# Optimization experiments

Hardware: AMD Instinct MI355X
Metric: run time of the kernel (lower is better)

The kernel has to match this reference:

```python
import jax, jax.numpy as jnp
import numpy as np

C = 80          # NUM_CLASSES
D = 8525        # total anchors over FPN levels (640 input: 80^2+40^2+20^2+10^2+5^2)
B = 64
EPS = 1e-6


def setup_inputs() -> dict:
    key = jax.random.key(0)
    ks = jax.random.split(key, 8)
    outs = jax.random.normal(ks[0], (B, D, C + 5), dtype=jnp.float32)
    grids = jax.random.uniform(ks[1], (D, 2), dtype=jnp.float32) * 640.0  # anchor centers (px)
    # --- build gres = [gcls(C), centerness(1), g_ltrb(4), mask_pp(1), mask_pos(1), pad(1)] ---
    labels = jax.random.randint(ks[2], (B, D), 0, C)
    mask_pos = (jax.random.uniform(ks[3], (B, D)) < 0.10).astype(jnp.float32)  # in-box positives
    mask_pp = (jax.random.uniform(ks[4], (B, D)) < 0.05).astype(jnp.float32)   # center-radius positives
    gcls = jax.nn.one_hot(labels, C, dtype=jnp.float32) * mask_pos[..., None]
    gcenterness = jax.random.uniform(ks[5], (B, D), dtype=jnp.float32)
    off = jax.random.uniform(ks[6], (B, D, 4), dtype=jnp.float32) * 64.0 + 1.0
    gx = grids[None, :, 0]
    gy = grids[None, :, 1]
    g_ltrb = jnp.stack([gx - off[..., 0], gy - off[..., 1],
                        gx + off[..., 2], gy + off[..., 3]], axis=-1)
    gres = jnp.concatenate([gcls,
                            gcenterness[..., None],
                            g_ltrb,
                            mask_pp[..., None],
                            mask_pos[..., None],
                            jnp.zeros((B, D, 1), jnp.float32)], axis=-1)  # [B, D, 88]
    nums_pos = jax.random.randint(ks[7], (B,), 1, 21).astype(jnp.int32)
    return {"outs": outs, "gres": gres, "grids": grids, "nums_pos": nums_pos}


def _giou(p, g):
    # elementwise GIoU on ltrb boxes, p/g: [..., 4]
    ix1 = jnp.maximum(p[..., 0], g[..., 0]); iy1 = jnp.maximum(p[..., 1], g[..., 1])
    ix2 = jnp.minimum(p[..., 2], g[..., 2]); iy2 = jnp.minimum(p[..., 3], g[..., 3])
    inter = jnp.clip(ix2 - ix1, 0.0) * jnp.clip(iy2 - iy1, 0.0)
    area_p = jnp.clip(p[..., 2] - p[..., 0], 0.0) * jnp.clip(p[..., 3] - p[..., 1], 0.0)
    area_g = jnp.clip(g[..., 2] - g[..., 0], 0.0) * jnp.clip(g[..., 3] - g[..., 1], 0.0)
    union = area_p + area_g - inter
    iou = inter / (union + EPS)
    cx1 = jnp.minimum(p[..., 0], g[..., 0]); cy1 = jnp.minimum(p[..., 1], g[..., 1])
    cx2 = jnp.maximum(p[..., 2], g[..., 2]); cy2 = jnp.maximum(p[..., 3], g[..., 3])
    c_area = (cx2 - cx1) * (cy2 - cy1)
    return iou - (c_area - union) / (c_area + EPS)


def reference(outs, gres, grids, nums_pos):
    np_f = nums_pos.astype(jnp.float32)
    # ---- cls: focal loss over all anchors ----
    pcls = jax.nn.sigmoid(outs[..., :C])          # [B, D, C]
    gcls = gres[..., :C]
    pos_m = (gcls == 1.0).astype(pcls.dtype)
    l_pos = -0.25 * (1.0 - pcls) ** 2 * jnp.log(pcls + EPS) * pos_m
    l_neg = -0.75 * pcls ** 2 * jnp.log(1.0 - pcls + EPS) * (1.0 - pos_m)
    l_cls_pos = jnp.mean(jnp.sum(l_pos, axis=(1, 2)) / np_f)
    l_cls_neg = jnp.mean(jnp.sum(l_neg, axis=(1, 2)) / np_f)
    # ---- conf: BCE(pconf, 1) over center-radius positives ----
    mask_pp = (gres[..., C + 5] == 1.0).astype(outs.dtype)
    pconf = jax.nn.sigmoid(outs[..., C])
    bce = -jnp.log(pconf + EPS)                    # target = ones
    l_conf = 5.0 * jnp.mean(jnp.sum(bce * mask_pp, axis=-1) / np_f)
    # ---- reg: masked GIoU over in-box positives ----
    mask_pos = (gres[..., C + 6] == 1.0).astype(outs.dtype)
    poff = outs[..., C + 1:C + 5]
    gxy = grids[None]                              # [1, D, 2]
    pboxes = jnp.concatenate([gxy - poff[..., :2], gxy + poff[..., 2:]], axis=-1)
    g_ltrb = gres[..., C + 1:C + 5]
    giou = _giou(pboxes, g_ltrb)                   # [B, D]
    gcenter = gres[..., C]
    n_pos = jnp.maximum(jnp.sum(mask_pos), 1.0)
    l_reg = 5.0 * jnp.sum((1.0 - giou) * gcenter * mask_pos) / n_pos
    return l_cls_pos + l_cls_neg + l_conf + l_reg
```

## Files before the change

kernel.cpp:

```cpp
#include <hip/hip_runtime.h>

namespace {

constexpr int   kC    = 80;
constexpr int   kD    = 8525;
constexpr int   kB    = 64;
constexpr float kEps  = 1e-6f;
constexpr int   kOC   = 85;
constexpr int   kGC   = 88;
constexpr int   kBlk  = 256;
constexpr int   kPB   = kD * kOC;
constexpr int   kSpb  = 32;
constexpr int   kRPS  = (kD + kSpb - 1) / kSpb;
constexpr int   kNT   = kB * kSpb;
constexpr int   kQW   = 12;

__device__ __forceinline__ float wave_reduce(float v) {
#pragma unroll
  for (int o = 32; o > 0; o >>= 1) v += __shfl_down(v, o, 64);
  return v;
}

__device__ __forceinline__ float fast_rcp(float x) {
  return __builtin_amdgcn_rcpf(x);
}

__device__ __forceinline__ float lneg_raw(float x) {
  const float p = fast_rcp(1.0f + __expf(-x));
  return p * p * __logf(1.0f - p + kEps);
}

__device__ __forceinline__ float lneg4(const float4 v) {
  return (lneg_raw(v.x) + lneg_raw(v.y)) + (lneg_raw(v.z) + lneg_raw(v.w));
}

__global__ __launch_bounds__(kBlk, 8) void floss_fused(
    const float* __restrict__ outs, const float* __restrict__ gres,
    const float* __restrict__ grids, const int* __restrict__ nums_pos,
    float* __restrict__ partials) {
  const int bid = blockIdx.x;
  const int tid = threadIdx.x;
  const int b   = bid >> 5;
  const int sb  = bid & 31;
  const int r0  = sb * kRPS;
  const int r1  = (r0 + kRPS < kD) ? r0 + kRPS : kD;
  const int nrows = r1 - r0;
  const float scale = fast_rcp(64.0f * (float)nums_pos[b]);

  __shared__ float s_q[kRPS * kQW];
  __shared__ int   s_cnt;
  __shared__ float sm[3][kBlk / 64];
  if (tid == 0) s_cnt = 0;

  float pm = 0.f, pr = 0.f, pn = 0.f;

  {
    const int gA = b * kPB + r0 * kOC;
    const int gB = gA + nrows * kOC;
    const int gv = (gA + 3) & ~3;
    const int nvec = (gB - gv) >> 2;
    const int gvend = gv + (nvec << 2);
    float a0 = 0.f, a1 = 0.f, a2 = 0.f, a3 = 0.f;
    if (tid < gv - gA)    a0 += lneg_raw(outs[gA + tid]);
    if (tid < gB - gvend) a1 += lneg_raw(outs[gvend + tid]);
    const float* pv = outs + gv;
    int v = tid;
    for (; v + 3 * kBlk < nvec; v += 4 * kBlk) {
      const float4 xa = *(const float4*)(pv + 4 * v);
      const float4 xb = *(const float4*)(pv + 4 * (v + kBlk));
      const float4 xc = *(const float4*)(pv + 4 * (v + 2 * kBlk));
      const float4 xd = *(const float4*)(pv + 4 * (v + 3 * kBlk));
      a0 += lneg4(xa);
      a1 += lneg4(xb);
      a2 += lneg4(xc);
      a3 += lneg4(xd);
    }
    for (; v < nvec; v += kBlk) a0 += lneg4(*(const float4*)(pv + 4 * v));
    pm += -0.75f * scale * ((a0 + a1) + (a2 + a3));
  }
  __syncthreads();

  for (int rl = tid; rl < nrows; rl += kBlk) {
    const int r   = r0 + rl;
    const int row = b * kD + r;
    const float* orow = outs + (size_t)row * kOC;
    const float x80 = orow[80], x81 = orow[81], x82 = orow[82],
                x83 = orow[83], x84 = orow[84];
    const size_t gb = (size_t)row * kGC;
    const float4 t0 = *(const float4*)(gres + gb + 80);
    const float4 t1 = *(const float4*)(gres + gb + 84);
    const float t5 = ((lneg_raw(x80) + lneg_raw(x81)) +
                     (lneg_raw(x82) + lneg_raw(x83))) + lneg_raw(x84);
    pm += 0.75f * scale * t5;
    if (t1.y == 1.0f) {
      const float pc = fast_rcp(1.0f + __expf(-x80));
      pm += -5.0f * __logf(pc + kEps) * scale;
    }
    if (t1.z == 1.0f) {
      pn += 1.0f;
      const int slot = atomicAdd(&s_cnt, 1);
      float* q = s_q + slot * kQW;
      q[0]  = t0.x;
      q[1]  = t0.y; q[2] = t0.z; q[3] = t0.w; q[4] = t1.x;
      q[5]  = x81;  q[6] = x82;  q[7] = x83;  q[8] = x84;
      q[9]  = grids[2 * r + 0];
      q[10] = grids[2 * r + 1];
      q[11] = __int_as_float(row);
    }
  }
  __syncthreads();

  {
    const int nq = s_cnt;
    const int hh = tid >> 5;
    const int h  = tid & 31;
    for (int e = hh; e < nq; e += 8) {
      const float* q = s_q + e * kQW;
      const int row = __float_as_int(q[11]);
      int cand = -1;
      if (h < 20) {
        const float4 v = *(const float4*)(gres + (size_t)row * kGC + 4 * h);
        if (v.x == 1.0f) cand = 4 * h;
        if (v.y == 1.0f) cand = 4 * h + 1;
        if (v.z == 1.0f) cand = 4 * h + 2;
        if (v.w == 1.0f) cand = 4 * h + 3;
      }
#pragma unroll
      for (int m = 16; m > 0; m >>= 1) {
        const int o = __shfl_xor(cand, m, 32);
        cand = (o > cand) ? o : cand;
      }
      if (h == 0 && cand >= 0) {
        const float x  = outs[(size_t)row * kOC + cand];
        const float p  = fast_rcp(1.0f + __expf(-x));
        const float om = 1.0f - p;
        const float lp = -0.25f * om * om * __logf(p + kEps);
        const float ln = -0.75f * p * p * __logf(om + kEps);
        pm += (lp - ln) * scale;
        const float gx = q[9], gy = q[10];
        const float p0 = gx - q[5], p1 = gy - q[6];
        const float p2 = gx + q[7], p3 = gy + q[8];
        const float g0 = q[1], g1 = q[2], g2 = q[3], g3 = q[4];
        const float iw = fmaxf(fminf(p2, g2) - fmaxf(p0, g0), 0.f);
        const float ih = fmaxf(fminf(p3, g3) - fmaxf(p1, g1), 0.f);
        const float inter = iw * ih;
        const float ap = fmaxf(p2 - p0, 0.f) * fmaxf(p3 - p1, 0.f);
        const float ag = fmaxf(g2 - g0, 0.f) * fmaxf(g3 - g1, 0.f);
        const float un = ap + ag - inter;
        const float iou = inter * fast_rcp(un + kEps);
        const float ca = (fmaxf(p2, g2) - fminf(p0, g0)) *
                         (fmaxf(p3, g3) - fminf(p1, g1));
        const float giou = iou - (ca - un) * fast_rcp(ca + kEps);
        pr += (1.0f - giou) * q[0];
      }
    }
  }

  const float vm = wave_reduce(pm);
  const float vr = wave_reduce(pr);
  const float vn = wave_reduce(pn);
  const int lane = tid & 63;
  const int w    = tid >> 6;
  if (lane == 0) { sm[0][w] = vm; sm[1][w] = vr; sm[2][w] = vn; }
  __syncthreads();
  if (tid == 0) {
    float m = 0.f, r = 0.f, n = 0.f;
#pragma unroll
    for (int j = 0; j < kBlk / 64; ++j) { m += sm[0][j]; r += sm[1][j]; n += sm[2][j]; }
    partials[bid * 3 + 0] = m;
    partials[bid * 3 + 1] = r;
    partials[bid * 3 + 2] = n;
  }
}

__global__ __launch_bounds__(kBlk) void floss_final(
    const float* __restrict__ partials, float* __restrict__ out) {
  float m = 0.f, r = 0.f, n = 0.f;
  for (int i = threadIdx.x; i < kNT; i += kBlk) {
    m += partials[i * 3 + 0];
    r += partials[i * 3 + 1];
    n += partials[i * 3 + 2];
  }
  __shared__ float sm[3][kBlk / 64];
  m = wave_reduce(m); r = wave_reduce(r); n = wave_reduce(n);
  const int lane = threadIdx.x & 63;
  const int w    = threadIdx.x >> 6;
  if (lane == 0) { sm[0][w] = m; sm[1][w] = r; sm[2][w] = n; }
  __syncthreads();
  if (threadIdx.x == 0) {
    float tm = 0.f, tr = 0.f, tn = 0.f;
#pragma unroll
    for (int j = 0; j < kBlk / 64; ++j) { tm += sm[0][j]; tr += sm[1][j]; tn += sm[2][j]; }
    out[0] = tm + 5.0f * tr / fmaxf(tn, 1.0f);
  }
}

}

extern "C" void kernel_launch(void* const* d_in, const int* in_sizes, int n_in,
                              void* d_out, int out_size, void* d_ws, size_t ws_size,
                              hipStream_t stream) {
  const float* outs     = (const float*)d_in[0];
  const float* gres     = (const float*)d_in[1];
  const float* grids    = (const float*)d_in[2];
  const int*   nums_pos = (const int*)d_in[3];
  float* partials = (float*)d_ws;

  floss_fused<<<kNT, kBlk, 0, stream>>>(outs, gres, grids, nums_pos, partials);
  floss_final<<<1, kBlk, 0, stream>>>(partials, (float*)d_out);
}
```

Before: 64.31 us.

## Split fused loss blocks into dense-streaming and per-row correction roles

Each block now takes one of two roles instead of doing everything. Streaming blocks (26 per batch) compute the dense negative focal term over an even flat chunk of the logits. Row blocks (6 per batch) handle the last five columns, the confidence term and the positive-anchor queue for GIoU and class correction. The queue entries shrink to 8 floats in a fixed 320-entry shared buffer, and the lane with h==20 reloads gres[80..83] rather than storing them in the queue. This removes the per-block barrier between the streaming and row phases and balances the streaming bandwidth. The risks are that the few long-running row blocks may set the tail, and that positives beyond the queue capacity would be silently dropped.

```diff
diff --git a/kernel.cpp b/kernel.cpp
--- a/kernel.cpp
+++ b/kernel.cpp
@@ -10,10 +10,17 @@
 constexpr int   kGC   = 88;
 constexpr int   kBlk  = 256;
 constexpr int   kPB   = kD * kOC;
-constexpr int   kSpb  = 32;
-constexpr int   kRPS  = (kD + kSpb - 1) / kSpb;
-constexpr int   kNT   = kB * kSpb;
-constexpr int   kQW   = 12;
+
+constexpr int   kRowPerB    = 6;
+constexpr int   kNRow       = kB * kRowPerB;
+constexpr int   kStreamPerB = 26;
+constexpr int   kNStream    = kB * kStreamPerB;
+constexpr int   kNT         = kNRow + kNStream;
+constexpr int   kChunk = (kPB + kStreamPerB - 1) / kStreamPerB;
+constexpr int   kRPB   = (kD + kRowPerB - 1) / kRowPerB;
+
+constexpr int   kQCap = 320;
+constexpr int   kQW   = 8;
 
 __device__ __forceinline__ float wave_reduce(float v) {
 #pragma unroll
@@ -40,23 +47,22 @@
     float* __restrict__ partials) {
   const int bid = blockIdx.x;
   const int tid = threadIdx.x;
-  const int b   = bid >> 5;
-  const int sb  = bid & 31;
-  const int r0  = sb * kRPS;
-  const int r1  = (r0 + kRPS < kD) ? r0 + kRPS : kD;
-  const int nrows = r1 - r0;
-  const float scale = fast_rcp(64.0f * (float)nums_pos[b]);
-
-  __shared__ float s_q[kRPS * kQW];
+
+  __shared__ float s_q[kQCap * kQW];
   __shared__ int   s_cnt;
   __shared__ float sm[3][kBlk / 64];
-  if (tid == 0) s_cnt = 0;
 
   float pm = 0.f, pr = 0.f, pn = 0.f;
 
-  {
-    const int gA = b * kPB + r0 * kOC;
-    const int gB = gA + nrows * kOC;
+  if (bid >= kNRow) {
+    const int sid = bid - kNRow;
+    const int b   = sid / kStreamPerB;
+    const int s   = sid - b * kStreamPerB;
+    const float scale = fast_rcp(64.0f * (float)nums_pos[b]);
+    const int e0 = s * kChunk;
+    const int e1 = (e0 + kChunk < kPB) ? e0 + kChunk : kPB;
+    const int gA = b * kPB + e0;
+    const int gB = b * kPB + e1;
     const int gv = (gA + 3) & ~3;
     const int nvec = (gB - gv) >> 2;
     const int gvend = gv + (nvec << 2);
@@ -76,71 +82,77 @@
       a3 += lneg4(xd);
     }
     for (; v < nvec; v += kBlk) a0 += lneg4(*(const float4*)(pv + 4 * v));
-    pm += -0.75f * scale * ((a0 + a1) + (a2 + a3));
-  }
-  __syncthreads();
-
-  for (int rl = tid; rl < nrows; rl += kBlk) {
-    const int r   = r0 + rl;
-    const int row = b * kD + r;
-    const float* orow = outs + (size_t)row * kOC;
-    const float x80 = orow[80], x81 = orow[81], x82 = orow[82],
-                x83 = orow[83], x84 = orow[84];
-    const size_t gb = (size_t)row * kGC;
-    const float4 t0 = *(const float4*)(gres + gb + 80);
-    const float4 t1 = *(const float4*)(gres + gb + 84);
-    const float t5 = ((lneg_raw(x80) + lneg_raw(x81)) +
-                     (lneg_raw(x82) + lneg_raw(x83))) + lneg_raw(x84);
-    pm += 0.75f * scale * t5;
-    if (t1.y == 1.0f) {
-      const float pc = fast_rcp(1.0f + __expf(-x80));
-      pm += -5.0f * __logf(pc + kEps) * scale;
+    pm = -0.75f * scale * ((a0 + a1) + (a2 + a3));
+  } else {
+    const int b  = bid / kRowPerB;
+    const int s  = bid - b * kRowPerB;
+    const int r0 = s * kRPB;
+    const int r1 = (r0 + kRPB < kD) ? r0 + kRPB : kD;
+    const float scale = fast_rcp(64.0f * (float)nums_pos[b]);
+
+    if (tid == 0) s_cnt = 0;
+    __syncthreads();
+
+    for (int r = r0 + tid; r < r1; r += kBlk) {
+      const int row = b * kD + r;
+      const float4 xt = *(const float4*)(outs + (size_t)row * kOC + 80);
+      const float  x84 = outs[(size_t)row * kOC + 84];
+      const float4 t1 = *(const float4*)(gres + (size_t)row * kGC + 84);
+      const float t5 = ((lneg_raw(xt.x) + lneg_raw(xt.y)) +
+                        (lneg_raw(xt.z) + lneg_raw(xt.w))) + lneg_raw(x84);
+      pm += 0.75f * scale * t5;
+      if (t1.y == 1.0f) {
+        const float pc = fast_rcp(1.0f + __expf(-xt.x));
+        pm += -5.0f * __logf(pc + kEps) * scale;
+      }
+      if (t1.z == 1.0f) {
+        pn += 1.0f;
+        const int slot = atomicAdd(&s_cnt, 1);
+        if (slot < kQCap) {
+          float* q = s_q + slot * kQW;
+          q[0] = __int_as_float(row);
+          q[1] = xt.y; q[2] = xt.z; q[3] = xt.w; q[4] = x84;
+          q[5] = grids[2 * r + 0];
+          q[6] = grids[2 * r + 1];
+          q[7] = t1.x;
+        }
+      }
     }
-    if (t1.z == 1.0f) {
-      pn += 1.0f;
-      const int slot = atomicAdd(&s_cnt, 1);
-      float* q = s_q + slot * kQW;
-      q[0]  = t0.x;
-      q[1]  = t0.y; q[2] = t0.z; q[3] = t0.w; q[4] = t1.x;
-      q[5]  = x81;  q[6] = x82;  q[7] = x83;  q[8] = x84;
-      q[9]  = grids[2 * r + 0];
-      q[10] = grids[2 * r + 1];
-      q[11] = __int_as_float(row);
-    }
-  }
-  __syncthreads();
-
-  {
-    const int nq = s_cnt;
+    __syncthreads();
+
+    const int nq = (s_cnt < kQCap) ? s_cnt : kQCap;
     const int hh = tid >> 5;
     const int h  = tid & 31;
     for (int e = hh; e < nq; e += 8) {
       const float* q = s_q + e * kQW;
-      const int row = __float_as_int(q[11]);
+      const int row = __float_as_int(q[0]);
       int cand = -1;
+      float4 v = make_float4(0.f, 0.f, 0.f, 0.f);
       if (h < 20) {
-        const float4 v = *(const float4*)(gres + (size_t)row * kGC + 4 * h);
+        v = *(const float4*)(gres + (size_t)row * kGC + 4 * h);
         if (v.x == 1.0f) cand = 4 * h;
         if (v.y == 1.0f) cand = 4 * h + 1;
         if (v.z == 1.0f) cand = 4 * h + 2;
         if (v.w == 1.0f) cand = 4 * h + 3;
+      } else if (h == 20) {
+        v = *(const float4*)(gres + (size_t)row * kGC + 80);
       }
 #pragma unroll
       for (int m = 16; m > 0; m >>= 1) {
         const int o = __shfl_xor(cand, m, 32);
         cand = (o > cand) ? o : cand;
       }
-      if (h == 0 && cand >= 0) {
+      if (h == 20 && cand >= 0) {
         const float x  = outs[(size_t)row * kOC + cand];
         const float p  = fast_rcp(1.0f + __expf(-x));
         const float om = 1.0f - p;
         const float lp = -0.25f * om * om * __logf(p + kEps);
         const float ln = -0.75f * p * p * __logf(om + kEps);
         pm += (lp - ln) * scale;
-        const float gx = q[9], gy = q[10];
-        const float p0 = gx - q[5], p1 = gy - q[6];
-        const float p2 = gx + q[7], p3 = gy + q[8];
-        const float g0 = q[1], g1 = q[2], g2 = q[3], g3 = q[4];
+        const float gx = q[5], gy = q[6];
+        const float p0 = gx - q[1], p1 = gy - q[2];
+        const float p2 = gx + q[3], p3 = gy + q[4];
+        const float g0 = v.y, g1 = v.z, g2 = v.w, g3 = q[7];
         const float iw = fmaxf(fminf(p2, g2) - fmaxf(p0, g0), 0.f);
         const float ih = fmaxf(fminf(p3, g3) - fmaxf(p1, g1), 0.f);
         const float inter = iw * ih;
@@ -151,7 +163,7 @@
         const float ca = (fmaxf(p2, g2) - fminf(p0, g0)) *
                          (fmaxf(p3, g3) - fminf(p1, g1));
         const float giou = iou - (ca - un) * fast_rcp(ca + kEps);
-        pr += (1.0f - giou) * q[0];
+        pr += (1.0f - giou) * v.x;
       }
     }
   }
```

After: 77.27 us. 1.2x slower.
